# Optimization experiments

Measured on AMD Instinct MI355X. Metric: run time of the kernel, lower is better.

Reference implementation:

```python
import jax, jax.numpy as jnp
import numpy as np

T, B = 64, 1024
DETER, STOC, EMB, ACT, MLP = 512, 64, 1024, 6, 512
MIN_STD = 0.1


def setup_inputs() -> dict:
    key = jax.random.key(0)
    ks = jax.random.split(key, 20)

    def lin(k, fan_in, fan_out):
        return jax.random.normal(k, (fan_in, fan_out), jnp.float32) / np.sqrt(fan_in)

    inp = {
        "actions": jax.random.normal(ks[0], (T, B, ACT), jnp.float32),
        "nonterminals": jnp.ones((T, B, 1), jnp.float32),
        "obs_embeddings": jax.random.normal(ks[1], (T, B, EMB), jnp.float32),
        "init_deter": jnp.zeros((B, DETER), jnp.float32),
        "init_stoc": jax.random.uniform(ks[2], (B, STOC), jnp.float32),
        "noise_prior": jax.random.uniform(ks[3], (T, B, STOC), jnp.float32),
        "noise_post": jax.random.uniform(ks[4], (T, B, STOC), jnp.float32),
        # fc_input
        "Wi": lin(ks[5], STOC + ACT, DETER),
        "bi": jnp.zeros((DETER,), jnp.float32),
        # GRUCell (torch layout: [3H, in], gate order r, z, n)
        "W_ih": jax.random.normal(ks[6], (3 * DETER, DETER), jnp.float32) / np.sqrt(DETER),
        "W_hh": jax.random.normal(ks[7], (3 * DETER, DETER), jnp.float32) / np.sqrt(DETER),
        "b_ih": jnp.zeros((3 * DETER,), jnp.float32),
        "b_hh": jnp.zeros((3 * DETER,), jnp.float32),
        # fc_prior
        "Wp1": lin(ks[8], DETER, MLP),
        "bp1": jnp.zeros((MLP,), jnp.float32),
        "Wp2": lin(ks[9], MLP, 2 * STOC),
        "bp2": jnp.zeros((2 * STOC,), jnp.float32),
        # fc_posterior
        "Wq1": lin(ks[10], DETER + EMB, MLP),
        "bq1": jnp.zeros((MLP,), jnp.float32),
        "Wq2": lin(ks[11], MLP, 2 * STOC),
        "bq2": jnp.zeros((2 * STOC,), jnp.float32),
    }
    return inp


def _rollout(actions, nonterminals, obs_embeddings, init_deter, init_stoc,
             noise_prior, noise_post, Wi, bi, W_ih, W_hh, b_ih, b_hh,
             Wp1, bp1, Wp2, bp2, Wq1, bq1, Wq2, bq2):
    def step(carry, inp):
        deter, stoc = carry
        a, nt, emb, eps_p, eps_q = inp
        # fc_input: Linear + ELU
        x = jax.nn.elu(jnp.concatenate([stoc * nt, a], axis=-1) @ Wi + bi)
        h = deter * nt
        # torch GRUCell
        gi = x @ W_ih.T + b_ih
        gh = h @ W_hh.T + b_hh
        ir, iz, inn = jnp.split(gi, 3, axis=-1)
        hr, hz, hn = jnp.split(gh, 3, axis=-1)
        r = jax.nn.sigmoid(ir + hr)
        z = jax.nn.sigmoid(iz + hz)
        n = jnp.tanh(inn + r * hn)
        deter_new = (1.0 - z) * n + z * h
        # prior head
        pr = jax.nn.elu(deter_new @ Wp1 + bp1) @ Wp2 + bp2
        pm, ps = jnp.split(pr, 2, axis=-1)
        ps = jax.nn.softplus(ps) + MIN_STD
        pstoc = pm + ps * eps_p  # uniform noise, as in RSSMState (torch.rand_like)
        # posterior head
        po = jax.nn.elu(jnp.concatenate([deter_new, emb], axis=-1) @ Wq1 + bq1) @ Wq2 + bq2
        qm, qs = jnp.split(po, 2, axis=-1)
        qs = jax.nn.softplus(qs) + MIN_STD
        qstoc = qm + qs * eps_q
        out = jnp.concatenate([deter_new, pm, ps, pstoc, qm, qs, qstoc], axis=-1)
        return (deter_new, qstoc), out

    _, outs = jax.lax.scan(step, (init_deter, init_stoc),
                           (actions, nonterminals, obs_embeddings, noise_prior, noise_post))
    return outs  # [T, B, DETER + 6*STOC]


def reference(actions, nonterminals, obs_embeddings, init_deter, init_stoc,
              noise_prior, noise_post, Wi, bi, W_ih, W_hh, b_ih, b_hh,
              Wp1, bp1, Wp2, bp2, Wq1, bq1, Wq2, bq2):
    return _rollout(actions, nonterminals, obs_embeddings, init_deter, init_stoc,
                    noise_prior, noise_post, Wi, bi, W_ih, W_hh, b_ih, b_hh,
                    Wp1, bp1, Wp2, bp2, Wq1, bq1, Wq2, bq2)
```

## Files before the change

### kernel.cpp

```cpp
#include <hip/hip_runtime.h>
#include <hip/hip_bf16.h>
#include <cstdint>

#define T_STEPS 64
#define BATCH   1024
#define DETER   512
#define STOC    64
#define EMB     1024
#define G3      1536
#define OUTD    896

#define DI __device__ __forceinline__

typedef __attribute__((ext_vector_type(8))) short bf8;
typedef __attribute__((ext_vector_type(4))) float f4;

DI float bf2f(short s) {
  union { uint32_t u; float f; } v; v.u = ((uint32_t)(uint16_t)s) << 16; return v.f;
}
DI short f2bf(float f) {
  union { float f; uint32_t u; } v; v.f = f;
  uint32_t r = (v.u + 0x7fffu + ((v.u >> 16) & 1u)) >> 16;
  return (short)(uint16_t)r;
}
DI float elu_f(float x)      { return x > 0.f ? x : expm1f(x); }
DI float sigm(float x)       { return 1.f / (1.f + expf(-x)); }
DI float softplus_f(float x) { return fmaxf(x, 0.f) + log1pf(expf(-fabsf(x))); }

DI bool is_f32(const void* nt) { return ((const uint32_t*)nt)[0] == 0x3F800000u; }
DI float gld(const void* p, size_t i, bool f) {
  return f ? ((const float*)p)[i] : bf2f(((const short*)p)[i]);
}
DI void gst(void* p, size_t i, float v, bool f) {
  if (f) ((float*)p)[i] = v; else ((short*)p)[i] = f2bf(v);
}

template<int BM, int BN, int WM, bool AF32, typename EPI>
DI void gemm_core(const void* Av, int lda, const short* Bp, int ldb, int K,
                  int m0, int n0, char* smem, int tid, EPI&& epi)
{
  constexpr int WN = 4 / WM;
  constexpr int SM = BM / 16 / WM;
  constexpr int SN = BN / 16 / WN;
  short* As = (short*)smem;
  short* Bs = As + BM * 32;
  int wave = tid >> 6, lane = tid & 63;
  int arow = (wave % WM) * (SM * 16), brow = (wave / WM) * (SN * 16);

  f4 acc[SM][SN] = {};

  for (int k0 = 0; k0 < K; k0 += 32) {
#pragma unroll
    for (int it = 0; it < (BM * 4) / 256; ++it) {
      int idx = it * 256 + tid;
      int r = idx >> 2, kc = (idx & 3) << 3;
      if (AF32) {
        const float* s = (const float*)Av + (size_t)(m0 + r) * lda + k0 + kc;
        f4 lo = *(const f4*)s, hi = *(const f4*)(s + 4);
        bf8 v;
#pragma unroll
        for (int j = 0; j < 4; ++j) { v[j] = f2bf(lo[j]); v[4 + j] = f2bf(hi[j]); }
        *(bf8*)&As[idx * 8] = v;
      } else {
        *(bf8*)&As[idx * 8] =
            *(const bf8*)((const short*)Av + (size_t)(m0 + r) * lda + k0 + kc);
      }
    }
#pragma unroll
    for (int it = 0; it < (BN * 4) / 256; ++it) {
      int idx = it * 256 + tid;
      int r = idx >> 2, kc = (idx & 3) << 3;
      *(bf8*)&Bs[idx * 8] = *(const bf8*)&Bp[(size_t)(n0 + r) * ldb + k0 + kc];
    }
    __syncthreads();

    bf8 af[SM], bfr[SN];
#pragma unroll
    for (int s = 0; s < SM; ++s)
      af[s] = *(const bf8*)&As[(arow + s * 16 + (lane & 15)) * 32 + ((lane >> 4) << 3)];
#pragma unroll
    for (int s = 0; s < SN; ++s)
      bfr[s] = *(const bf8*)&Bs[(brow + s * 16 + (lane & 15)) * 32 + ((lane >> 4) << 3)];
#pragma unroll
    for (int sm = 0; sm < SM; ++sm)
#pragma unroll
      for (int sn = 0; sn < SN; ++sn)
        acc[sm][sn] = __builtin_amdgcn_mfma_f32_16x16x32_bf16(af[sm], bfr[sn], acc[sm][sn], 0, 0, 0);
    __syncthreads();
  }
  epi(acc, m0 + arow, n0 + brow, lane);
}

__global__ __launch_bounds__(256) void k_prep(
    const void* __restrict__ Wi,  const void* __restrict__ Wp1,
    const void* __restrict__ Wq1, const void* __restrict__ Wp2,
    const void* __restrict__ Wq2, const void* __restrict__ Wih,
    const void* __restrict__ Whh, const void* __restrict__ nt,
    short* __restrict__ WiT, short* __restrict__ WpT, short* __restrict__ WqT,
    short* __restrict__ Wp2T, short* __restrict__ Wq2T,
    short* __restrict__ Wihc, short* __restrict__ Whhc)
{
  bool f = is_f32(nt);
  int idx = blockIdx.x * 256 + threadIdx.x;
  if (idx < 512 * 96) {
    int n = idx / 96, k = idx % 96;
    WiT[idx] = (k < 70) ? f2bf(gld(Wi, (size_t)k * 512 + n, f)) : (short)0;
    return;
  }
  idx -= 512 * 96;
  if (idx < 512 * 512) {
    int n = idx >> 9, k = idx & 511;
    WpT[idx] = f2bf(gld(Wp1, (size_t)k * 512 + n, f));
    return;
  }
  idx -= 512 * 512;
  if (idx < 512 * 1536) {
    int n = idx / 1536, k = idx % 1536;
    WqT[idx] = f2bf(gld(Wq1, (size_t)k * 512 + n, f));
    return;
  }
  idx -= 512 * 1536;
  if (idx < 128 * 512) {
    int n = idx >> 9, k = idx & 511;
    Wp2T[idx] = f2bf(gld(Wp2, (size_t)k * 128 + n, f));
    return;
  }
  idx -= 128 * 512;
  if (idx < 128 * 512) {
    int n = idx >> 9, k = idx & 511;
    Wq2T[idx] = f2bf(gld(Wq2, (size_t)k * 128 + n, f));
    return;
  }
  idx -= 128 * 512;
  if (idx < G3 * 512) { Wihc[idx] = f2bf(gld(Wih, idx, f)); return; }
  idx -= G3 * 512;
  if (idx < G3 * 512) { Whhc[idx] = f2bf(gld(Whh, idx, f)); }
}

__global__ __launch_bounds__(256) void k_init(
    const void* __restrict__ init_deter, const void* __restrict__ init_stoc,
    const void* __restrict__ nt, const void* __restrict__ actions,
    short* __restrict__ Ax, short* __restrict__ hbf, float* __restrict__ hf32)
{
  bool f = is_f32(nt);
  int idx = blockIdx.x * 256 + threadIdx.x;
  if (idx < BATCH * 96) {
    int b = idx / 96, k = idx % 96;
    float nt0 = gld(nt, b, f);
    float v;
    if (k < 64)      v = gld(init_stoc, (size_t)b * 64 + k, f) * nt0;
    else if (k < 70) v = gld(actions, (size_t)b * 6 + (k - 64), f);
    else             v = 0.f;
    Ax[idx] = f2bf(v);
  } else {
    int j = idx - BATCH * 96;
    if (j < BATCH * DETER) {
      int b = j >> 9;
      float v = gld(init_deter, j, f) * gld(nt, b, f);
      hbf[j]  = f2bf(v);
      hf32[j] = v;
    }
  }
}

__global__ __launch_bounds__(256) void k_phase1(
    const short* __restrict__ Ax, const short* __restrict__ WiT, const void* __restrict__ bi,
    const short* __restrict__ hbf, const short* __restrict__ Whhc, const void* __restrict__ bhh,
    const void* __restrict__ emb, int t, const short* __restrict__ WqT,
    const void* __restrict__ nt,
    short* __restrict__ x, short* __restrict__ gh, short* __restrict__ hq2)
{
  extern __shared__ char smem[];
  bool f = is_f32(nt);
  int tid = threadIdx.x, b = blockIdx.x;
  if (b < 32) {
    int m0 = (b >> 2) * 128, n0 = (b & 3) * 128;
    gemm_core<128, 128, 2, false>(Ax, 96, WiT, 96, 96, m0, n0, smem, tid,
      [&](auto& acc, int rb, int cb, int lane) {
        int q = lane >> 4, li = lane & 15;
#pragma unroll
        for (int sm = 0; sm < 4; ++sm)
#pragma unroll
          for (int sn = 0; sn < 4; ++sn)
#pragma unroll
            for (int i = 0; i < 4; ++i) {
              int r = rb + sm * 16 + q * 4 + i, c = cb + sn * 16 + li;
              x[(size_t)r * 512 + c] = f2bf(elu_f(acc[sm][sn][i] + gld(bi, c, f)));
            }
      });
  } else if (b < 224) {
    int r = b - 32;
    int m0 = (r / 24) * 128, n0 = (r % 24) * 64;
    gemm_core<128, 64, 2, false>(hbf, 512, Whhc, 512, 512, m0, n0, smem, tid,
      [&](auto& acc, int rb, int cb, int lane) {
        int q = lane >> 4, li = lane & 15;
#pragma unroll
        for (int sm = 0; sm < 4; ++sm)
#pragma unroll
          for (int sn = 0; sn < 2; ++sn)
#pragma unroll
            for (int i = 0; i < 4; ++i) {
              int rr = rb + sm * 16 + q * 4 + i, c = cb + sn * 16 + li;
              gh[(size_t)rr * G3 + c] = f2bf(acc[sm][sn][i] + gld(bhh, c, f));
            }
      });
  } else {
    int r = b - 224;
    int m0 = (r / 8) * 64, n0 = (r % 8) * 64;
    size_t eoff = (size_t)t * BATCH * EMB;
    auto epi = [&](auto& acc, int rb, int cb, int lane) {
      int q = lane >> 4, li = lane & 15;
#pragma unroll
      for (int sm = 0; sm < 2; ++sm)
#pragma unroll
        for (int sn = 0; sn < 2; ++sn)
#pragma unroll
          for (int i = 0; i < 4; ++i) {
            int rr = rb + sm * 16 + q * 4 + i, c = cb + sn * 16 + li;
            hq2[(size_t)rr * 512 + c] = f2bf(acc[sm][sn][i]);
          }
    };
    if (f) gemm_core<64, 64, 2, true >((const void*)((const float*)emb + eoff), 1024,
                                       WqT + 512, 1536, 1024, m0, n0, smem, tid, epi);
    else   gemm_core<64, 64, 2, false>((const void*)((const short*)emb + eoff), 1024,
                                       WqT + 512, 1536, 1024, m0, n0, smem, tid, epi);
  }
}

__global__ __launch_bounds__(256) void k_gru(
    const short* __restrict__ x, const short* __restrict__ Wihc, const void* __restrict__ bih,
    const short* __restrict__ gh, const void* __restrict__ nt, int t,
    short* __restrict__ hbf, float* __restrict__ hf32,
    short* __restrict__ dbf, void* __restrict__ outv)
{
  extern __shared__ char smem[];
  bool f = is_f32(nt);
  short* As = (short*)smem;
  short* Bs = As + 128 * 32;
  int tid = threadIdx.x, lane = tid & 63, wave = tid >> 6;
  int m0 = (blockIdx.x >> 3) * 128, n0 = (blockIdx.x & 7) * 64;
  int arow = (wave & 1) * 64, brow = (wave >> 1) * 32;

  f4 acc[3][4][2] = {};

  for (int k0 = 0; k0 < 512; k0 += 32) {
#pragma unroll
    for (int it = 0; it < 2; ++it) {
      int idx = it * 256 + tid;
      *(bf8*)&As[idx * 8] = *(const bf8*)&x[(size_t)(m0 + (idx >> 2)) * 512 + k0 + ((idx & 3) << 3)];
    }
#pragma unroll
    for (int g = 0; g < 3; ++g) {
      int idx = tid;
      *(bf8*)&Bs[g * 2048 + idx * 8] =
          *(const bf8*)&Wihc[(size_t)(n0 + g * 512 + (idx >> 2)) * 512 + k0 + ((idx & 3) << 3)];
    }
    __syncthreads();

    bf8 af[4];
#pragma unroll
    for (int s = 0; s < 4; ++s)
      af[s] = *(const bf8*)&As[(arow + s * 16 + (lane & 15)) * 32 + ((lane >> 4) << 3)];
#pragma unroll
    for (int g = 0; g < 3; ++g)
#pragma unroll
      for (int sn = 0; sn < 2; ++sn) {
        bf8 bfr = *(const bf8*)&Bs[g * 2048 + (brow + sn * 16 + (lane & 15)) * 32 + ((lane >> 4) << 3)];
#pragma unroll
        for (int sm = 0; sm < 4; ++sm)
          acc[g][sm][sn] = __builtin_amdgcn_mfma_f32_16x16x32_bf16(af[sm], bfr, acc[g][sm][sn], 0, 0, 0);
      }
    __syncthreads();
  }

  int q = lane >> 4, li = lane & 15;
#pragma unroll
  for (int sm = 0; sm < 4; ++sm)
#pragma unroll
    for (int sn = 0; sn < 2; ++sn)
#pragma unroll
      for (int i = 0; i < 4; ++i) {
        int r = m0 + arow + sm * 16 + q * 4 + i;
        int c = n0 + brow + sn * 16 + li;
        float ir  = acc[0][sm][sn][i] + gld(bih, c, f);
        float iz  = acc[1][sm][sn][i] + gld(bih, 512 + c, f);
        float in_ = acc[2][sm][sn][i] + gld(bih, 1024 + c, f);
        size_t gb = (size_t)r * G3;
        float hr = bf2f(gh[gb + c]);
        float hz = bf2f(gh[gb + 512 + c]);
        float hn = bf2f(gh[gb + 1024 + c]);
        float h  = hf32[(size_t)r * 512 + c];
        float rr = sigm(ir + hr);
        float zz = sigm(iz + hz);
        float nn = tanhf(in_ + rr * hn);
        float dn = (1.f - zz) * nn + zz * h;
        gst(outv, ((size_t)t * BATCH + r) * OUTD + c, dn, f);
        dbf[(size_t)r * 512 + c] = f2bf(dn);
        if (t < T_STEPS - 1) {
          float hv = dn * gld(nt, (size_t)(t + 1) * BATCH + r, f);
          hbf[(size_t)r * 512 + c]  = f2bf(hv);
          hf32[(size_t)r * 512 + c] = hv;
        }
      }
}

__global__ __launch_bounds__(256) void k_phase4(
    const short* __restrict__ dbf, const short* __restrict__ WpT, const void* __restrict__ bp1,
    const short* __restrict__ WqT, const void* __restrict__ bq1,
    const short* __restrict__ hq2, const void* __restrict__ nt,
    short* __restrict__ hp, short* __restrict__ hq)
{
  extern __shared__ char smem[];
  bool f = is_f32(nt);
  int tid = threadIdx.x, b = blockIdx.x;
  if (b < 64) {
    int m0 = (b / 8) * 128, n0 = (b % 8) * 64;
    gemm_core<128, 64, 2, false>(dbf, 512, WpT, 512, 512, m0, n0, smem, tid,
      [&](auto& acc, int rb, int cb, int lane) {
        int q = lane >> 4, li = lane & 15;
#pragma unroll
        for (int sm = 0; sm < 4; ++sm)
#pragma unroll
          for (int sn = 0; sn < 2; ++sn)
#pragma unroll
            for (int i = 0; i < 4; ++i) {
              int rr = rb + sm * 16 + q * 4 + i, c = cb + sn * 16 + li;
              hp[(size_t)rr * 512 + c] = f2bf(elu_f(acc[sm][sn][i] + gld(bp1, c, f)));
            }
      });
  } else {
    int r = b - 64;
    int m0 = (r / 8) * 128, n0 = (r % 8) * 64;
    gemm_core<128, 64, 2, false>(dbf, 512, WqT, 1536, 512, m0, n0, smem, tid,
      [&](auto& acc, int rb, int cb, int lane) {
        int q = lane >> 4, li = lane & 15;
#pragma unroll
        for (int sm = 0; sm < 4; ++sm)
#pragma unroll
          for (int sn = 0; sn < 2; ++sn)
#pragma unroll
            for (int i = 0; i < 4; ++i) {
              int rr = rb + sm * 16 + q * 4 + i, c = cb + sn * 16 + li;
              float v = acc[sm][sn][i] + bf2f(hq2[(size_t)rr * 512 + c]) + gld(bq1, c, f);
              hq[(size_t)rr * 512 + c] = f2bf(elu_f(v));
            }
      });
  }
}

__global__ __launch_bounds__(256) void k_heads(
    const short* __restrict__ hp, const short* __restrict__ hq,
    const short* __restrict__ Wp2T, const short* __restrict__ Wq2T,
    const void* __restrict__ bp2, const void* __restrict__ bq2,
    const void* __restrict__ noise_p, const void* __restrict__ noise_q,
    const void* __restrict__ nt, const void* __restrict__ actions, int t,
    void* __restrict__ outv, short* __restrict__ Ax)
{
  extern __shared__ char smem[];
  bool f = is_f32(nt);
  int tid = threadIdx.x;
  int head = blockIdx.x & 1;
  int bm   = blockIdx.x >> 1;
  const short* Asrc = head ? hq : hp;
  const short* Bsrc = head ? Wq2T : Wp2T;
  const void* b2    = head ? bq2 : bp2;
  const void* eps   = head ? noise_q : noise_p;
  int obase = head ? 704 : 512;

  gemm_core<64, 128, 4, false>(Asrc, 512, Bsrc, 512, 512, bm * 64, 0, smem, tid,
    [&](auto& acc, int rb, int cb, int lane) {
      int q = lane >> 4, li = lane & 15;
      (void)cb;
#pragma unroll
      for (int sn = 0; sn < 4; ++sn)
#pragma unroll
        for (int i = 0; i < 4; ++i) {
          int r = rb + q * 4 + i;
          int c = sn * 16 + li;
          float m  = acc[0][sn][i]     + gld(b2, c, f);
          float sp = acc[0][sn + 4][i] + gld(b2, 64 + c, f);
          float s  = softplus_f(sp) + 0.1f;
          float e  = gld(eps, ((size_t)t * BATCH + r) * 64 + c, f);
          float st = m + s * e;
          size_t ob = ((size_t)t * BATCH + r) * OUTD + obase;
          gst(outv, ob + c,       m,  f);
          gst(outv, ob + 64 + c,  s,  f);
          gst(outv, ob + 128 + c, st, f);
          if (head && t < T_STEPS - 1)
            Ax[(size_t)r * 96 + c] = f2bf(st * gld(nt, (size_t)(t + 1) * BATCH + r, f));
        }
    });

  if (head == 0 && t < T_STEPS - 1) {
    for (int idx = tid; idx < 64 * 32; idx += 256) {
      int r = bm * 64 + (idx >> 5);
      int c = 64 + (idx & 31);
      float v = (c < 70) ? gld(actions, ((size_t)(t + 1) * BATCH + r) * 6 + (c - 64), f) : 0.f;
      Ax[(size_t)r * 96 + c] = f2bf(v);
    }
  }
}

extern "C" void kernel_launch(void* const* d_in, const int* in_sizes, int n_in,
                              void* d_out, int out_size, void* d_ws, size_t ws_size,
                              hipStream_t stream)
{
  const void* actions    = d_in[0];
  const void* nonterm    = d_in[1];
  const void* emb        = d_in[2];
  const void* init_deter = d_in[3];
  const void* init_stoc  = d_in[4];
  const void* noise_p    = d_in[5];
  const void* noise_q    = d_in[6];
  const void* Wi  = d_in[7];
  const void* bi  = d_in[8];
  const void* Wih = d_in[9];
  const void* Whh = d_in[10];
  const void* bih = d_in[11];
  const void* bhh = d_in[12];
  const void* Wp1 = d_in[13];
  const void* bp1 = d_in[14];
  const void* Wp2 = d_in[15];
  const void* bp2 = d_in[16];
  const void* Wq1 = d_in[17];
  const void* bq1 = d_in[18];
  const void* Wq2 = d_in[19];
  const void* bq2 = d_in[20];

  char* ws = (char*)d_ws;
  short* WiT  = (short*)(ws + 0);
  short* WpT  = (short*)(ws + 98304);
  short* WqT  = (short*)(ws + 622592);
  short* Wp2T = (short*)(ws + 2195456);
  short* Wq2T = (short*)(ws + 2326528);
  short* Wihc = (short*)(ws + 2457600);
  short* Whhc = (short*)(ws + 4030464);
  short* Ax   = (short*)(ws + 5603328);
  short* x    = (short*)(ws + 5799936);
  short* dbf  = (short*)(ws + 6848512);
  short* hbf  = (short*)(ws + 7897088);
  short* hp   = (short*)(ws + 8945664);
  short* hq   = (short*)(ws + 9994240);
  short* gh   = (short*)(ws + 11042816);
  short* hq2  = (short*)(ws + 14188544);
  float* hf32 = (float*)(ws + 15237120);

  (void)in_sizes; (void)n_in; (void)out_size;
  if (ws_size < 17334272) return;

  k_prep<<<10944, 256, 0, stream>>>(Wi, Wp1, Wq1, Wp2, Wq2, Wih, Whh, nonterm,
                                    WiT, WpT, WqT, Wp2T, Wq2T, Wihc, Whhc);
  k_init<<<2432, 256, 0, stream>>>(init_deter, init_stoc, nonterm, actions, Ax, hbf, hf32);

  for (int t = 0; t < T_STEPS; ++t) {
    k_phase1<<<352, 256, 16384, stream>>>(Ax, WiT, bi, hbf, Whhc, bhh, emb, t, WqT,
                                          nonterm, x, gh, hq2);
    k_gru<<<64, 256, 20480, stream>>>(x, Wihc, bih, gh, nonterm, t, hbf, hf32, dbf, d_out);
    k_phase4<<<128, 256, 12288, stream>>>(dbf, WpT, bp1, WqT, bq1, hq2, nonterm, hp, hq);
    k_heads<<<32, 256, 12288, stream>>>(hp, hq, Wp2T, Wq2T, bp2, bq2,
                                        noise_p, noise_q, nonterm, actions, t, d_out, Ax);
  }
}
```

Before: 7.658 ms.

## Fuse per-step kernels into one persistent cooperative kernel with grid barriers

Replaces the four kernel launches per timestep with a single persistent cooperative kernel of 512 blocks that moves through two phases per step, separated by a software grid barrier built on an atomic counter. The work is regrouped: the GRU block fuses the input projection with the gate math, each head block fuses both MLP layers with the next step's input projection, and the Whh GEMM for step t+1 overlaps with the heads of step t. This is meant to remove launch overhead and the global-memory round-trips for the intermediate hp and hq buffers. In exchange it relies on all blocks being co-resident, uses smaller tiles that may underuse the MFMA units, and falls back to separate per-phase launches if the cooperative launch fails.

```diff
diff --git a/kernel.cpp b/kernel.cpp
--- a/kernel.cpp
+++ b/kernel.cpp
@@ -1,5 +1,4 @@
 #include <hip/hip_runtime.h>
-#include <hip/hip_bf16.h>
 #include <cstdint>
 
 #define T_STEPS 64
@@ -9,6 +8,7 @@
 #define EMB     1024
 #define G3      1536
 #define OUTD    896
+#define NBLK    512
 
 #define DI __device__ __forceinline__
 
@@ -33,6 +33,28 @@
 }
 DI void gst(void* p, size_t i, float v, bool f) {
   if (f) ((float*)p)[i] = v; else ((short*)p)[i] = f2bf(v);
+}
+
+struct Params {
+  const void *actions, *nonterm, *emb;
+  const void *bi, *bih, *bhh, *bp1, *bp2, *bq1, *bq2, *noise_p, *noise_q;
+  const short *WiT, *WpT, *WqT, *Wp2T, *Wq2T, *Wihc, *Whhc, *Ax0;
+  short *x, *dbf, *hbf, *gh, *hq2;
+  float *hf32;
+  unsigned *bar;
+  void *outv;
+};
+
+DI void gsync(unsigned* bar, unsigned target, int tid) {
+  __threadfence();
+  __syncthreads();
+  if (tid == 0) {
+    atomicAdd(bar, 1u);
+    while (__hip_atomic_load(bar, __ATOMIC_RELAXED, __HIP_MEMORY_SCOPE_AGENT) < target)
+      __builtin_amdgcn_s_sleep(1);
+  }
+  __syncthreads();
+  __threadfence();
 }
 
 template<int BM, int BN, int WM, bool AF32, typename EPI>
@@ -50,27 +72,33 @@
   f4 acc[SM][SN] = {};
 
   for (int k0 = 0; k0 < K; k0 += 32) {
-#pragma unroll
-    for (int it = 0; it < (BM * 4) / 256; ++it) {
+    constexpr int ACH = BM * 4;
+#pragma unroll
+    for (int it = 0; it < (ACH + 255) / 256; ++it) {
       int idx = it * 256 + tid;
-      int r = idx >> 2, kc = (idx & 3) << 3;
-      if (AF32) {
-        const float* s = (const float*)Av + (size_t)(m0 + r) * lda + k0 + kc;
-        f4 lo = *(const f4*)s, hi = *(const f4*)(s + 4);
-        bf8 v;
-#pragma unroll
-        for (int j = 0; j < 4; ++j) { v[j] = f2bf(lo[j]); v[4 + j] = f2bf(hi[j]); }
-        *(bf8*)&As[idx * 8] = v;
-      } else {
-        *(bf8*)&As[idx * 8] =
-            *(const bf8*)((const short*)Av + (size_t)(m0 + r) * lda + k0 + kc);
-      }
-    }
-#pragma unroll
-    for (int it = 0; it < (BN * 4) / 256; ++it) {
+      if (ACH % 256 == 0 || idx < ACH) {
+        int r = idx >> 2, kc = (idx & 3) << 3;
+        if (AF32) {
+          const float* s = (const float*)Av + (size_t)(m0 + r) * lda + k0 + kc;
+          f4 lo = *(const f4*)s, hi = *(const f4*)(s + 4);
+          bf8 v;
+#pragma unroll
+          for (int j = 0; j < 4; ++j) { v[j] = f2bf(lo[j]); v[4 + j] = f2bf(hi[j]); }
+          *(bf8*)&As[idx * 8] = v;
+        } else {
+          *(bf8*)&As[idx * 8] =
+              *(const bf8*)((const short*)Av + (size_t)(m0 + r) * lda + k0 + kc);
+        }
+      }
+    }
+    constexpr int BCH = BN * 4;
+#pragma unroll
+    for (int it = 0; it < (BCH + 255) / 256; ++it) {
       int idx = it * 256 + tid;
-      int r = idx >> 2, kc = (idx & 3) << 3;
-      *(bf8*)&Bs[idx * 8] = *(const bf8*)&Bp[(size_t)(n0 + r) * ldb + k0 + kc];
+      if (BCH % 256 == 0 || idx < BCH) {
+        int r = idx >> 2, kc = (idx & 3) << 3;
+        *(bf8*)&Bs[idx * 8] = *(const bf8*)&Bp[(size_t)(n0 + r) * ldb + k0 + kc];
+      }
     }
     __syncthreads();
 
@@ -89,6 +117,307 @@
     __syncthreads();
   }
   epi(acc, m0 + arow, n0 + brow, lane);
+}
+
+DI void gru_block(const Params& P, int bid, int t, bool f, char* smem, int tid)
+{
+  short* As = (short*)smem;
+  short* Bs = As + 1024;
+  int lane = tid & 63, wave = tid >> 6;
+  int m0 = (bid >> 3) * 32, n0 = (bid & 7) * 64;
+  int arow = (wave & 1) * 16, bcol = (wave >> 1) * 32;
+  int q = lane >> 4, li = lane & 15;
+
+  f4 acc[3][2] = {};
+  for (int k0 = 0; k0 < 512; k0 += 32) {
+    if (tid < 128)
+      *(bf8*)&As[tid * 8] =
+          *(const bf8*)&P.x[(size_t)(m0 + (tid >> 2)) * 512 + k0 + ((tid & 3) << 3)];
+#pragma unroll
+    for (int g = 0; g < 3; ++g)
+      *(bf8*)&Bs[g * 2048 + tid * 8] =
+          *(const bf8*)&P.Wihc[(size_t)(n0 + g * 512 + (tid >> 2)) * 512 + k0 + ((tid & 3) << 3)];
+    __syncthreads();
+    bf8 af = *(const bf8*)&As[(arow + li) * 32 + (q << 3)];
+#pragma unroll
+    for (int g = 0; g < 3; ++g)
+#pragma unroll
+      for (int sn = 0; sn < 2; ++sn) {
+        bf8 bf_ = *(const bf8*)&Bs[g * 2048 + (bcol + sn * 16 + li) * 32 + (q << 3)];
+        acc[g][sn] = __builtin_amdgcn_mfma_f32_16x16x32_bf16(af, bf_, acc[g][sn], 0, 0, 0);
+      }
+    __syncthreads();
+  }
+#pragma unroll
+  for (int sn = 0; sn < 2; ++sn)
+#pragma unroll
+    for (int i = 0; i < 4; ++i) {
+      int r = m0 + arow + q * 4 + i;
+      int c = n0 + bcol + sn * 16 + li;
+      float ir  = acc[0][sn][i] + gld(P.bih, c, f);
+      float iz  = acc[1][sn][i] + gld(P.bih, 512 + c, f);
+      float in_ = acc[2][sn][i] + gld(P.bih, 1024 + c, f);
+      size_t gb = (size_t)r * G3;
+      float hr = bf2f(P.gh[gb + c]);
+      float hz = bf2f(P.gh[gb + 512 + c]);
+      float hn = bf2f(P.gh[gb + 1024 + c]);
+      float h  = P.hf32[(size_t)r * 512 + c];
+      float rr = sigm(ir + hr);
+      float zz = sigm(iz + hz);
+      float nn = tanhf(in_ + rr * hn);
+      float dn = (1.f - zz) * nn + zz * h;
+      gst(P.outv, ((size_t)t * BATCH + r) * OUTD + c, dn, f);
+      P.dbf[(size_t)r * 512 + c] = f2bf(dn);
+      if (t < T_STEPS - 1) {
+        float hv = dn * gld(P.nonterm, (size_t)(t + 1) * BATCH + r, f);
+        P.hbf[(size_t)r * 512 + c]  = f2bf(hv);
+        P.hf32[(size_t)r * 512 + c] = hv;
+      }
+    }
+}
+
+template<bool POST>
+DI void head_block(const Params& P, int tile, int t, bool f, char* smem, int tid)
+{
+  const short* W1 = POST ? P.WqT : P.WpT;
+  const int ldw1  = POST ? 1536 : 512;
+  const void* b1  = POST ? P.bq1 : P.bp1;
+  const short* W2 = POST ? P.Wq2T : P.Wp2T;
+  const void* b2  = POST ? P.bq2 : P.bp2;
+  const void* eps = POST ? P.noise_q : P.noise_p;
+  const int obase = POST ? 704 : 512;
+
+  int lane = tid & 63, wave = tid >> 6;
+  int q = lane >> 4, li = lane & 15;
+  int r0 = tile * 16;
+  short* Bs  = (short*)smem;
+  short* Asm = (short*)(smem + 32768);
+  short* hl  = (short*)(smem + 33792);
+  float* po  = (float*)(smem + 50176);
+  short* axl = (short*)(smem + 58624);
+
+  f4 a1[8] = {};
+  for (int k0 = 0; k0 < 512; k0 += 32) {
+    if (tid < 64)
+      *(bf8*)&Asm[tid * 8] =
+          *(const bf8*)&P.dbf[(size_t)(r0 + (tid >> 2)) * 512 + k0 + ((tid & 3) << 3)];
+#pragma unroll
+    for (int it = 0; it < 8; ++it) {
+      int idx = it * 256 + tid;
+      *(bf8*)&Bs[idx * 8] = *(const bf8*)&W1[(size_t)(idx >> 2) * ldw1 + k0 + ((idx & 3) << 3)];
+    }
+    __syncthreads();
+    bf8 af = *(const bf8*)&Asm[li * 32 + (q << 3)];
+#pragma unroll
+    for (int sn = 0; sn < 8; ++sn) {
+      bf8 bf_ = *(const bf8*)&Bs[(wave * 128 + sn * 16 + li) * 32 + (q << 3)];
+      a1[sn] = __builtin_amdgcn_mfma_f32_16x16x32_bf16(af, bf_, a1[sn], 0, 0, 0);
+    }
+    __syncthreads();
+  }
+#pragma unroll
+  for (int sn = 0; sn < 8; ++sn)
+#pragma unroll
+    for (int i = 0; i < 4; ++i) {
+      int r = q * 4 + i, c = wave * 128 + sn * 16 + li;
+      float v = a1[sn][i] + gld(b1, c, f);
+      if (POST) v += bf2f(P.hq2[(size_t)(r0 + r) * 512 + c]);
+      int bo = (r * 1024 + c * 2) ^ ((r & 7) << 4);
+      *(short*)((char*)hl + bo) = f2bf(elu_f(v));
+    }
+  __syncthreads();
+
+  f4 a2[2] = {};
+  for (int k0 = 0; k0 < 512; k0 += 32) {
+#pragma unroll
+    for (int it = 0; it < 2; ++it) {
+      int idx = it * 256 + tid;
+      *(bf8*)&Bs[idx * 8] = *(const bf8*)&W2[(size_t)(idx >> 2) * 512 + k0 + ((idx & 3) << 3)];
+    }
+    __syncthreads();
+    int bo = (li * 1024 + (k0 + (q << 3)) * 2) ^ ((li & 7) << 4);
+    bf8 af = *(const bf8*)((char*)hl + bo);
+#pragma unroll
+    for (int sn = 0; sn < 2; ++sn) {
+      bf8 bf_ = *(const bf8*)&Bs[(wave * 32 + sn * 16 + li) * 32 + (q << 3)];
+      a2[sn] = __builtin_amdgcn_mfma_f32_16x16x32_bf16(af, bf_, a2[sn], 0, 0, 0);
+    }
+    __syncthreads();
+  }
+#pragma unroll
+  for (int sn = 0; sn < 2; ++sn)
+#pragma unroll
+    for (int i = 0; i < 4; ++i)
+      po[(q * 4 + i) * 132 + wave * 32 + sn * 16 + li] = a2[sn][i];
+  __syncthreads();
+
+  {
+    int r = tid >> 4, g = tid & 15;
+    float ntn = (POST && t < T_STEPS - 1)
+                ? gld(P.nonterm, (size_t)(t + 1) * BATCH + r0 + r, f) : 0.f;
+#pragma unroll
+    for (int j = 0; j < 4; ++j) {
+      int c = g * 4 + j;
+      float m  = po[r * 132 + c]      + gld(b2, c, f);
+      float sp = po[r * 132 + 64 + c] + gld(b2, 64 + c, f);
+      float s  = softplus_f(sp) + 0.1f;
+      float e  = gld(eps, ((size_t)t * BATCH + r0 + r) * 64 + c, f);
+      float st = m + s * e;
+      size_t ob = ((size_t)t * BATCH + r0 + r) * OUTD + obase;
+      gst(P.outv, ob + c,       m,  f);
+      gst(P.outv, ob + 64 + c,  s,  f);
+      gst(P.outv, ob + 128 + c, st, f);
+      if (POST && t < T_STEPS - 1) axl[r * 104 + c] = f2bf(st * ntn);
+    }
+  }
+
+  if (POST && t < T_STEPS - 1) {
+    for (int idx = tid; idx < 16 * 40; idx += 256) {
+      int r = idx / 40, c = 64 + idx % 40;
+      axl[r * 104 + c] =
+          (c < 70) ? f2bf(gld(P.actions, ((size_t)(t + 1) * BATCH + r0 + r) * 6 + (c - 64), f))
+                   : (short)0;
+    }
+    __syncthreads();
+    f4 a3[8] = {};
+    for (int k0 = 0; k0 < 96; k0 += 32) {
+#pragma unroll
+      for (int it = 0; it < 8; ++it) {
+        int idx = it * 256 + tid;
+        *(bf8*)&Bs[idx * 8] = *(const bf8*)&P.WiT[(size_t)(idx >> 2) * 96 + k0 + ((idx & 3) << 3)];
+      }
+      __syncthreads();
+      bf8 af = *(const bf8*)&axl[li * 104 + k0 + (q << 3)];
+#pragma unroll
+      for (int sn = 0; sn < 8; ++sn) {
+        bf8 bf_ = *(const bf8*)&Bs[(wave * 128 + sn * 16 + li) * 32 + (q << 3)];
+        a3[sn] = __builtin_amdgcn_mfma_f32_16x16x32_bf16(af, bf_, a3[sn], 0, 0, 0);
+      }
+      __syncthreads();
+    }
+#pragma unroll
+    for (int sn = 0; sn < 8; ++sn)
+#pragma unroll
+      for (int i = 0; i < 4; ++i) {
+        int r = r0 + q * 4 + i, c = wave * 128 + sn * 16 + li;
+        P.x[(size_t)r * 512 + c] = f2bf(elu_f(a3[sn][i] + gld(P.bi, c, f)));
+      }
+  }
+}
+
+DI void prologue(const Params& P, int bid, bool f, char* smem, int tid)
+{
+  if (bid < 384) {
+    int m0 = (bid / 24) * 64, n0 = (bid % 24) * 64;
+    gemm_core<64, 64, 2, false>(P.hbf, 512, P.Whhc, 512, 512, m0, n0, smem, tid,
+      [&](auto& acc, int rb, int cb, int lane) {
+        int q = lane >> 4, li = lane & 15;
+#pragma unroll
+        for (int sm = 0; sm < 2; ++sm)
+#pragma unroll
+          for (int sn = 0; sn < 2; ++sn)
+#pragma unroll
+            for (int i = 0; i < 4; ++i) {
+              int rr = rb + sm * 16 + q * 4 + i, c = cb + sn * 16 + li;
+              P.gh[(size_t)rr * G3 + c] = f2bf(acc[sm][sn][i] + gld(P.bhh, c, f));
+            }
+      });
+  } else {
+    int r = bid - 384;
+    int m0 = (r >> 3) * 64, n0 = (r & 7) * 64;
+    gemm_core<64, 64, 2, false>(P.Ax0, 96, P.WiT, 96, 96, m0, n0, smem, tid,
+      [&](auto& acc, int rb, int cb, int lane) {
+        int q = lane >> 4, li = lane & 15;
+#pragma unroll
+        for (int sm = 0; sm < 2; ++sm)
+#pragma unroll
+          for (int sn = 0; sn < 2; ++sn)
+#pragma unroll
+            for (int i = 0; i < 4; ++i) {
+              int rr = rb + sm * 16 + q * 4 + i, c = cb + sn * 16 + li;
+              P.x[(size_t)rr * 512 + c] = f2bf(elu_f(acc[sm][sn][i] + gld(P.bi, c, f)));
+            }
+      });
+  }
+}
+
+DI void phaseA(const Params& P, int bid, int t, bool f, char* smem, int tid)
+{
+  if (bid < 256) {
+    gru_block(P, bid, t, f, smem, tid);
+  } else {
+    int r = bid - 256;
+    int m0 = (r >> 3) * 32, n0 = (r & 7) * 64;
+    auto epi = [&](auto& acc, int rb, int cb, int lane) {
+      int q = lane >> 4, li = lane & 15;
+#pragma unroll
+      for (int sn = 0; sn < 2; ++sn)
+#pragma unroll
+        for (int i = 0; i < 4; ++i)
+          P.hq2[(size_t)(rb + q * 4 + i) * 512 + cb + sn * 16 + li] = f2bf(acc[0][sn][i]);
+    };
+    if (f) gemm_core<32, 64, 2, true >((const void*)((const float*)P.emb + (size_t)t * BATCH * EMB),
+                                       1024, P.WqT + 512, 1536, 1024, m0, n0, smem, tid, epi);
+    else   gemm_core<32, 64, 2, false>((const void*)((const short*)P.emb + (size_t)t * BATCH * EMB),
+                                       1024, P.WqT + 512, 1536, 1024, m0, n0, smem, tid, epi);
+  }
+}
+
+DI void phaseB(const Params& P, int bid, int t, bool f, char* smem, int tid)
+{
+  if (bid < 384) {
+    if (t < T_STEPS - 1) {
+      int m0 = (bid / 24) * 64, n0 = (bid % 24) * 64;
+      gemm_core<64, 64, 2, false>(P.hbf, 512, P.Whhc, 512, 512, m0, n0, smem, tid,
+        [&](auto& acc, int rb, int cb, int lane) {
+          int q = lane >> 4, li = lane & 15;
+#pragma unroll
+          for (int sm = 0; sm < 2; ++sm)
+#pragma unroll
+            for (int sn = 0; sn < 2; ++sn)
+#pragma unroll
+              for (int i = 0; i < 4; ++i) {
+                int rr = rb + sm * 16 + q * 4 + i, c = cb + sn * 16 + li;
+                P.gh[(size_t)rr * G3 + c] = f2bf(acc[sm][sn][i] + gld(P.bhh, c, f));
+              }
+        });
+    }
+  } else if (bid < 448) {
+    head_block<false>(P, bid - 384, t, f, smem, tid);
+  } else {
+    head_block<true >(P, bid - 448, t, f, smem, tid);
+  }
+}
+
+__global__ __launch_bounds__(256, 2) void k_roll(Params P)
+{
+  __shared__ __align__(16) char smem[62208];
+  bool f = is_f32(P.nonterm);
+  int tid = threadIdx.x, bid = blockIdx.x;
+  unsigned tgt = NBLK;
+
+  prologue(P, bid, f, smem, tid);
+  gsync(P.bar, tgt, tid);
+
+  for (int t = 0; t < T_STEPS; ++t) {
+    phaseA(P, bid, t, f, smem, tid);
+    tgt += NBLK; gsync(P.bar, tgt, tid);
+    phaseB(P, bid, t, f, smem, tid);
+    tgt += NBLK; gsync(P.bar, tgt, tid);
+  }
+}
+
+__global__ __launch_bounds__(256) void k_pro(Params P) {
+  __shared__ __align__(16) char smem[62208];
+  prologue(P, blockIdx.x, is_f32(P.nonterm), smem, threadIdx.x);
+}
+__global__ __launch_bounds__(256) void k_pA(Params P, int t) {
+  __shared__ __align__(16) char smem[62208];
+  phaseA(P, blockIdx.x, t, is_f32(P.nonterm), smem, threadIdx.x);
+}
+__global__ __launch_bounds__(256) void k_pB(Params P, int t) {
+  __shared__ __align__(16) char smem[62208];
+  phaseB(P, blockIdx.x, t, is_f32(P.nonterm), smem, threadIdx.x);
 }
 
 __global__ __launch_bounds__(256) void k_prep(
@@ -140,8 +469,10 @@
 __global__ __launch_bounds__(256) void k_init(
     const void* __restrict__ init_deter, const void* __restrict__ init_stoc,
     const void* __restrict__ nt, const void* __restrict__ actions,
-    short* __restrict__ Ax, short* __restrict__ hbf, float* __restrict__ hf32)
-{
+    short* __restrict__ Ax, short* __restrict__ hbf, float* __restrict__ hf32,
+    unsigned* __restrict__ bar)
+{
+  if (blockIdx.x == 0 && threadIdx.x == 0) *bar = 0u;
   bool f = is_f32(nt);
   int idx = blockIdx.x * 256 + threadIdx.x;
   if (idx < BATCH * 96) {
@@ -159,244 +490,6 @@
       float v = gld(init_deter, j, f) * gld(nt, b, f);
       hbf[j]  = f2bf(v);
       hf32[j] = v;
-    }
-  }
-}
-
-__global__ __launch_bounds__(256) void k_phase1(
-    const short* __restrict__ Ax, const short* __restrict__ WiT, const void* __restrict__ bi,
-    const short* __restrict__ hbf, const short* __restrict__ Whhc, const void* __restrict__ bhh,
-    const void* __restrict__ emb, int t, const short* __restrict__ WqT,
-    const void* __restrict__ nt,
-    short* __restrict__ x, short* __restrict__ gh, short* __restrict__ hq2)
-{
-  extern __shared__ char smem[];
-  bool f = is_f32(nt);
-  int tid = threadIdx.x, b = blockIdx.x;
-  if (b < 32) {
-    int m0 = (b >> 2) * 128, n0 = (b & 3) * 128;
-    gemm_core<128, 128, 2, false>(Ax, 96, WiT, 96, 96, m0, n0, smem, tid,
-      [&](auto& acc, int rb, int cb, int lane) {
-        int q = lane >> 4, li = lane & 15;
-#pragma unroll
-        for (int sm = 0; sm < 4; ++sm)
-#pragma unroll
-          for (int sn = 0; sn < 4; ++sn)
-#pragma unroll
-            for (int i = 0; i < 4; ++i) {
-              int r = rb + sm * 16 + q * 4 + i, c = cb + sn * 16 + li;
-              x[(size_t)r * 512 + c] = f2bf(elu_f(acc[sm][sn][i] + gld(bi, c, f)));
-            }
-      });
-  } else if (b < 224) {
-    int r = b - 32;
-    int m0 = (r / 24) * 128, n0 = (r % 24) * 64;
-    gemm_core<128, 64, 2, false>(hbf, 512, Whhc, 512, 512, m0, n0, smem, tid,
-      [&](auto& acc, int rb, int cb, int lane) {
-        int q = lane >> 4, li = lane & 15;
-#pragma unroll
-        for (int sm = 0; sm < 4; ++sm)
-#pragma unroll
-          for (int sn = 0; sn < 2; ++sn)
-#pragma unroll
-            for (int i = 0; i < 4; ++i) {
-              int rr = rb + sm * 16 + q * 4 + i, c = cb + sn * 16 + li;
-              gh[(size_t)rr * G3 + c] = f2bf(acc[sm][sn][i] + gld(bhh, c, f));
-            }
-      });
-  } else {
-    int r = b - 224;
-    int m0 = (r / 8) * 64, n0 = (r % 8) * 64;
-    size_t eoff = (size_t)t * BATCH * EMB;
-    auto epi = [&](auto& acc, int rb, int cb, int lane) {
-      int q = lane >> 4, li = lane & 15;
-#pragma unroll
-      for (int sm = 0; sm < 2; ++sm)
-#pragma unroll
-        for (int sn = 0; sn < 2; ++sn)
-#pragma unroll
-          for (int i = 0; i < 4; ++i) {
-            int rr = rb + sm * 16 + q * 4 + i, c = cb + sn * 16 + li;
-            hq2[(size_t)rr * 512 + c] = f2bf(acc[sm][sn][i]);
-          }
-    };
-    if (f) gemm_core<64, 64, 2, true >((const void*)((const float*)emb + eoff), 1024,
-                                       WqT + 512, 1536, 1024, m0, n0, smem, tid, epi);
-    else   gemm_core<64, 64, 2, false>((const void*)((const short*)emb + eoff), 1024,
-                                       WqT + 512, 1536, 1024, m0, n0, smem, tid, epi);
-  }
-}
-
-__global__ __launch_bounds__(256) void k_gru(
-    const short* __restrict__ x, const short* __restrict__ Wihc, const void* __restrict__ bih,
-    const short* __restrict__ gh, const void* __restrict__ nt, int t,
-    short* __restrict__ hbf, float* __restrict__ hf32,
-    short* __restrict__ dbf, void* __restrict__ outv)
-{
-  extern __shared__ char smem[];
-  bool f = is_f32(nt);
-  short* As = (short*)smem;
-  short* Bs = As + 128 * 32;
-  int tid = threadIdx.x, lane = tid & 63, wave = tid >> 6;
-  int m0 = (blockIdx.x >> 3) * 128, n0 = (blockIdx.x & 7) * 64;
-  int arow = (wave & 1) * 64, brow = (wave >> 1) * 32;
-
-  f4 acc[3][4][2] = {};
-
-  for (int k0 = 0; k0 < 512; k0 += 32) {
-#pragma unroll
-    for (int it = 0; it < 2; ++it) {
-      int idx = it * 256 + tid;
-      *(bf8*)&As[idx * 8] = *(const bf8*)&x[(size_t)(m0 + (idx >> 2)) * 512 + k0 + ((idx & 3) << 3)];
-    }
-#pragma unroll
-    for (int g = 0; g < 3; ++g) {
-      int idx = tid;
-      *(bf8*)&Bs[g * 2048 + idx * 8] =
-          *(const bf8*)&Wihc[(size_t)(n0 + g * 512 + (idx >> 2)) * 512 + k0 + ((idx & 3) << 3)];
-    }
-    __syncthreads();
-
-    bf8 af[4];
-#pragma unroll
-    for (int s = 0; s < 4; ++s)
-      af[s] = *(const bf8*)&As[(arow + s * 16 + (lane & 15)) * 32 + ((lane >> 4) << 3)];
-#pragma unroll
-    for (int g = 0; g < 3; ++g)
-#pragma unroll
-      for (int sn = 0; sn < 2; ++sn) {
-        bf8 bfr = *(const bf8*)&Bs[g * 2048 + (brow + sn * 16 + (lane & 15)) * 32 + ((lane >> 4) << 3)];
-#pragma unroll
-        for (int sm = 0; sm < 4; ++sm)
-          acc[g][sm][sn] = __builtin_amdgcn_mfma_f32_16x16x32_bf16(af[sm], bfr, acc[g][sm][sn], 0, 0, 0);
-      }
-    __syncthreads();
-  }
-
-  int q = lane >> 4, li = lane & 15;
-#pragma unroll
-  for (int sm = 0; sm < 4; ++sm)
-#pragma unroll
-    for (int sn = 0; sn < 2; ++sn)
-#pragma unroll
-      for (int i = 0; i < 4; ++i) {
-        int r = m0 + arow + sm * 16 + q * 4 + i;
-        int c = n0 + brow + sn * 16 + li;
-        float ir  = acc[0][sm][sn][i] + gld(bih, c, f);
-        float iz  = acc[1][sm][sn][i] + gld(bih, 512 + c, f);
-        float in_ = acc[2][sm][sn][i] + gld(bih, 1024 + c, f);
-        size_t gb = (size_t)r * G3;
-        float hr = bf2f(gh[gb + c]);
-        float hz = bf2f(gh[gb + 512 + c]);
-        float hn = bf2f(gh[gb + 1024 + c]);
-        float h  = hf32[(size_t)r * 512 + c];
-        float rr = sigm(ir + hr);
-        float zz = sigm(iz + hz);
-        float nn = tanhf(in_ + rr * hn);
-        float dn = (1.f - zz) * nn + zz * h;
-        gst(outv, ((size_t)t * BATCH + r) * OUTD + c, dn, f);
-        dbf[(size_t)r * 512 + c] = f2bf(dn);
-        if (t < T_STEPS - 1) {
-          float hv = dn * gld(nt, (size_t)(t + 1) * BATCH + r, f);
-          hbf[(size_t)r * 512 + c]  = f2bf(hv);
-          hf32[(size_t)r * 512 + c] = hv;
-        }
-      }
-}
-
-__global__ __launch_bounds__(256) void k_phase4(
-    const short* __restrict__ dbf, const short* __restrict__ WpT, const void* __restrict__ bp1,
-    const short* __restrict__ WqT, const void* __restrict__ bq1,
-    const short* __restrict__ hq2, const void* __restrict__ nt,
-    short* __restrict__ hp, short* __restrict__ hq)
-{
-  extern __shared__ char smem[];
-  bool f = is_f32(nt);
-  int tid = threadIdx.x, b = blockIdx.x;
-  if (b < 64) {
-    int m0 = (b / 8) * 128, n0 = (b % 8) * 64;
-    gemm_core<128, 64, 2, false>(dbf, 512, WpT, 512, 512, m0, n0, smem, tid,
-      [&](auto& acc, int rb, int cb, int lane) {
-        int q = lane >> 4, li = lane & 15;
-#pragma unroll
-        for (int sm = 0; sm < 4; ++sm)
-#pragma unroll
-          for (int sn = 0; sn < 2; ++sn)
-#pragma unroll
-            for (int i = 0; i < 4; ++i) {
-              int rr = rb + sm * 16 + q * 4 + i, c = cb + sn * 16 + li;
-              hp[(size_t)rr * 512 + c] = f2bf(elu_f(acc[sm][sn][i] + gld(bp1, c, f)));
-            }
-      });
-  } else {
-    int r = b - 64;
-    int m0 = (r / 8) * 128, n0 = (r % 8) * 64;
-    gemm_core<128, 64, 2, false>(dbf, 512, WqT, 1536, 512, m0, n0, smem, tid,
-      [&](auto& acc, int rb, int cb, int lane) {
-        int q = lane >> 4, li = lane & 15;
-#pragma unroll
-        for (int sm = 0; sm < 4; ++sm)
-#pragma unroll
-          for (int sn = 0; sn < 2; ++sn)
-#pragma unroll
-            for (int i = 0; i < 4; ++i) {
-              int rr = rb + sm * 16 + q * 4 + i, c = cb + sn * 16 + li;
-              float v = acc[sm][sn][i] + bf2f(hq2[(size_t)rr * 512 + c]) + gld(bq1, c, f);
-              hq[(size_t)rr * 512 + c] = f2bf(elu_f(v));
-            }
-      });
-  }
-}
-
-__global__ __launch_bounds__(256) void k_heads(
-    const short* __restrict__ hp, const short* __restrict__ hq,
-    const short* __restrict__ Wp2T, const short* __restrict__ Wq2T,
-    const void* __restrict__ bp2, const void* __restrict__ bq2,
-    const void* __restrict__ noise_p, const void* __restrict__ noise_q,
-    const void* __restrict__ nt, const void* __restrict__ actions, int t,
-    void* __restrict__ outv, short* __restrict__ Ax)
-{
-  extern __shared__ char smem[];
-  bool f = is_f32(nt);
-  int tid = threadIdx.x;
-  int head = blockIdx.x & 1;
-  int bm   = blockIdx.x >> 1;
-  const short* Asrc = head ? hq : hp;
-  const short* Bsrc = head ? Wq2T : Wp2T;
-  const void* b2    = head ? bq2 : bp2;
-  const void* eps   = head ? noise_q : noise_p;
-  int obase = head ? 704 : 512;
-
-  gemm_core<64, 128, 4, false>(Asrc, 512, Bsrc, 512, 512, bm * 64, 0, smem, tid,
-    [&](auto& acc, int rb, int cb, int lane) {
-      int q = lane >> 4, li = lane & 15;
-      (void)cb;
-#pragma unroll
-      for (int sn = 0; sn < 4; ++sn)
-#pragma unroll
-        for (int i = 0; i < 4; ++i) {
-          int r = rb + q * 4 + i;
-          int c = sn * 16 + li;
-          float m  = acc[0][sn][i]     + gld(b2, c, f);
-          float sp = acc[0][sn + 4][i] + gld(b2, 64 + c, f);
-          float s  = softplus_f(sp) + 0.1f;
-          float e  = gld(eps, ((size_t)t * BATCH + r) * 64 + c, f);
-          float st = m + s * e;
-          size_t ob = ((size_t)t * BATCH + r) * OUTD + obase;
-          gst(outv, ob + c,       m,  f);
-          gst(outv, ob + 64 + c,  s,  f);
-          gst(outv, ob + 128 + c, st, f);
-          if (head && t < T_STEPS - 1)
-            Ax[(size_t)r * 96 + c] = f2bf(st * gld(nt, (size_t)(t + 1) * BATCH + r, f));
-        }
-    });
-
-  if (head == 0 && t < T_STEPS - 1) {
-    for (int idx = tid; idx < 64 * 32; idx += 256) {
-      int r = bm * 64 + (idx >> 5);
-      int c = 64 + (idx & 31);
-      float v = (c < 70) ? gld(actions, ((size_t)(t + 1) * BATCH + r) * 6 + (c - 64), f) : 0.f;
-      Ax[(size_t)r * 96 + c] = f2bf(v);
     }
   }
 }
@@ -435,29 +528,41 @@
   short* Wq2T = (short*)(ws + 2326528);
   short* Wihc = (short*)(ws + 2457600);
   short* Whhc = (short*)(ws + 4030464);
-  short* Ax   = (short*)(ws + 5603328);
+  short* Ax0  = (short*)(ws + 5603328);
   short* x    = (short*)(ws + 5799936);
   short* dbf  = (short*)(ws + 6848512);
   short* hbf  = (short*)(ws + 7897088);
-  short* hp   = (short*)(ws + 8945664);
-  short* hq   = (short*)(ws + 9994240);
-  short* gh   = (short*)(ws + 11042816);
-  short* hq2  = (short*)(ws + 14188544);
-  float* hf32 = (float*)(ws + 15237120);
+  short* gh   = (short*)(ws + 8945664);
+  short* hq2  = (short*)(ws + 12091392);
+  float* hf32 = (float*)(ws + 13139968);
+  unsigned* bar = (unsigned*)(ws + 15237120);
 
   (void)in_sizes; (void)n_in; (void)out_size;
-  if (ws_size < 17334272) return;
+  if (ws_size < 15237184) return;
 
   k_prep<<<10944, 256, 0, stream>>>(Wi, Wp1, Wq1, Wp2, Wq2, Wih, Whh, nonterm,
                                     WiT, WpT, WqT, Wp2T, Wq2T, Wihc, Whhc);
-  k_init<<<2432, 256, 0, stream>>>(init_deter, init_stoc, nonterm, actions, Ax, hbf, hf32);
-
-  for (int t = 0; t < T_STEPS; ++t) {
-    k_phase1<<<352, 256, 16384, stream>>>(Ax, WiT, bi, hbf, Whhc, bhh, emb, t, WqT,
-                                          nonterm, x, gh, hq2);
-    k_gru<<<64, 256, 20480, stream>>>(x, Wihc, bih, gh, nonterm, t, hbf, hf32, dbf, d_out);
-    k_phase4<<<128, 256, 12288, stream>>>(dbf, WpT, bp1, WqT, bq1, hq2, nonterm, hp, hq);
-    k_heads<<<32, 256, 12288, stream>>>(hp, hq, Wp2T, Wq2T, bp2, bq2,
-                                        noise_p, noise_q, nonterm, actions, t, d_out, Ax);
-  }
-}
+  k_init<<<2432, 256, 0, stream>>>(init_deter, init_stoc, nonterm, actions,
+                                   Ax0, hbf, hf32, bar);
+
+  Params P;
+  P.actions = actions; P.nonterm = nonterm; P.emb = emb;
+  P.bi = bi; P.bih = bih; P.bhh = bhh;
+  P.bp1 = bp1; P.bp2 = bp2; P.bq1 = bq1; P.bq2 = bq2;
+  P.noise_p = noise_p; P.noise_q = noise_q;
+  P.WiT = WiT; P.WpT = WpT; P.WqT = WqT; P.Wp2T = Wp2T; P.Wq2T = Wq2T;
+  P.Wihc = Wihc; P.Whhc = Whhc; P.Ax0 = Ax0;
+  P.x = x; P.dbf = dbf; P.hbf = hbf; P.gh = gh; P.hq2 = hq2;
+  P.hf32 = hf32; P.bar = bar; P.outv = d_out;
+
+  void* kargs[] = { (void*)&P };
+  hipError_t e = hipLaunchCooperativeKernel((const void*)k_roll, dim3(NBLK), dim3(256),
+                                            kargs, 0, stream);
+  if (e != hipSuccess) {
+    k_pro<<<NBLK, 256, 0, stream>>>(P);
+    for (int t = 0; t < T_STEPS; ++t) {
+      k_pA<<<NBLK, 256, 0, stream>>>(P, t);
+      k_pB<<<NBLK, 256, 0, stream>>>(P, t);
+    }
+  }
+}
```

Measured after the change: 22.46 ms. 2.93x slower.
